# Performance work log

Hardware: AMD Instinct MI355X
Metric: run time of the kernel (lower is better)

The kernel has to match this reference:

```python
import jax, jax.numpy as jnp
import numpy as np

B = 65536
D_MODEL = 2048
N_EXPERTS = 64
TOP_K = 8
AUX_COEF = 0.01


def setup_inputs() -> dict:
    key = jax.random.key(0)
    kx, kw = jax.random.split(key)
    x = jax.random.normal(kx, (B, D_MODEL), dtype=jnp.float32)
    # nn.Linear(d_model, n_experts, bias=False); stored here as (d_model, n_experts)
    W = jax.random.normal(kw, (D_MODEL, N_EXPERTS), dtype=jnp.float32) / np.sqrt(D_MODEL).astype(np.float32)
    expert_bias = jnp.zeros((N_EXPERTS,), dtype=jnp.float32)
    return {"x": x, "W": W, "expert_bias": expert_bias}


def reference(x, W, expert_bias):
    # router logits: (B, n_experts)
    logits = x @ W
    # topk on bias-shifted logits (aux-loss-free balancing bias)
    biased = logits + expert_bias
    _, indices = jax.lax.top_k(biased, TOP_K)              # (B, top_k) int32
    # softmax over the UNbiased logits of the selected experts
    selected = jnp.take_along_axis(logits, indices, axis=-1)  # (B, top_k)
    gates_topk = jax.nn.softmax(selected, axis=-1)
    # scatter gate weights into sparse (B, n_experts) tensor
    rows = jnp.arange(logits.shape[0])[:, None]
    gates = jnp.zeros_like(logits).at[rows, indices].set(gates_topk)
    # aux load-balance loss (training mode): fraction routed * mean prob
    f_i = (gates > 0).astype(logits.dtype).mean(axis=0)       # (n_experts,)
    P_i = jax.nn.softmax(logits, axis=-1).mean(axis=0)        # (n_experts,)
    aux_loss = AUX_COEF * N_EXPERTS * jnp.sum(f_i * P_i)
    return gates, indices, aux_loss
```

## Files before the change

kernel.cpp:

```cpp
#include <hip/hip_runtime.h>
#include <cstdint>
#include <cstddef>

typedef __attribute__((ext_vector_type(8))) short short8;
typedef __attribute__((ext_vector_type(4))) float f32x4;

#define B_ROWS 65536
#define DMODEL 2048
#define NEXP 64
#define TOPK 8
#define THREADS 256
#define ROWS_PER_BLK 128
#define NBLK (B_ROWS / ROWS_PER_BLK)
#define NKS (DMODEL / 32)
#define SLAB 72
#define GOFF ((size_t)B_ROWS * NEXP)
#define AUX_OFF (GOFF + (size_t)B_ROWS * TOPK)
#define WS_FRAG_OFF 65536

__device__ __forceinline__ unsigned short bf16_rne(float v, float* back) {
  unsigned u = __float_as_uint(v);
  unsigned r = (u + 0x7FFFu + ((u >> 16) & 1u)) >> 16;
  *back = __uint_as_float(r << 16);
  return (unsigned short)r;
}

__global__ __launch_bounds__(256) void router_prep(
    const float* __restrict__ W, unsigned short* __restrict__ frag)
{
  const int ks = blockIdx.x;
  const int tid = threadIdx.x;
  const int nt = tid >> 6;
  const int lane = tid & 63;
  const int krow = ks * 32 + (lane >> 4) * 8;
  const int col = nt * 16 + (lane & 15);
  short8 hv, mv, lv;
#pragma unroll
  for (int j = 0; j < 8; ++j) {
    float v = W[(size_t)(krow + j) * NEXP + col];
    float fh, fm, fl;
    unsigned short h = bf16_rne(v, &fh);
    float r = v - fh;
    unsigned short m = bf16_rne(r, &fm);
    float r2 = r - fm;
    unsigned short l = bf16_rne(r2, &fl);
    hv[j] = (short)h; mv[j] = (short)m; lv[j] = (short)l;
  }
  size_t base = (size_t)(ks * 4 + nt) * 3 * 512 + lane * 8;
  *(short8*)(frag + base)        = hv;
  *(short8*)(frag + base + 512)  = mv;
  *(short8*)(frag + base + 1024) = lv;
}

__device__ __forceinline__ void cvt3(float4 a, float4 b,
                                     short8* H, short8* M, short8* L) {
  float f[8] = {a.x, a.y, a.z, a.w, b.x, b.y, b.z, b.w};
#pragma unroll
  for (int j = 0; j < 8; ++j) {
    float fh, fm, fl;
    unsigned short h = bf16_rne(f[j], &fh);
    float r = f[j] - fh;
    unsigned short m = bf16_rne(r, &fm);
    float r2 = r - fm;
    unsigned short l = bf16_rne(r2, &fl);
    (*H)[j] = (short)h; (*M)[j] = (short)m; (*L)[j] = (short)l;
  }
}

#define MFMA __builtin_amdgcn_mfma_f32_16x16x32_bf16

__global__ __launch_bounds__(THREADS, 2) void router_main(
    const float* __restrict__ x, const float* __restrict__ bias,
    const unsigned short* __restrict__ frag, float* __restrict__ out,
    float* __restrict__ ws)
{
  __shared__ __align__(16) float lds[ROWS_PER_BLK * SLAB + 256];

  const int tid = threadIdx.x;
  const int lane = tid & 63;
  const int w = tid >> 6;
  const size_t row0 = (size_t)blockIdx.x * ROWS_PER_BLK;

  f32x4 acc[2][4];
#pragma unroll
  for (int m = 0; m < 2; ++m)
#pragma unroll
    for (int nt = 0; nt < 4; ++nt) acc[m][nt] = (f32x4){0.f, 0.f, 0.f, 0.f};

  const float* xp0 = x + (row0 + (size_t)w * 32 + (lane & 15)) * DMODEL
                   + (lane >> 4) * 8;
  const float* xp1 = xp0 + (size_t)16 * DMODEL;
  const short8* fb = (const short8*)frag;

  for (int ks = 0; ks < NKS; ++ks) {
    float4 a00 = *(const float4*)(xp0 + ks * 32);
    float4 a01 = *(const float4*)(xp0 + ks * 32 + 4);
    float4 a10 = *(const float4*)(xp1 + ks * 32);
    float4 a11 = *(const float4*)(xp1 + ks * 32 + 4);
    short8 Bh[4], Bm[4], Bl[4];
#pragma unroll
    for (int nt = 0; nt < 4; ++nt) {
      size_t fb0 = (size_t)(ks * 4 + nt) * 3 * 64 + lane;
      Bh[nt] = fb[fb0];
      Bm[nt] = fb[fb0 + 64];
      Bl[nt] = fb[fb0 + 128];
    }
    short8 Ah0, Am0, Al0, Ah1, Am1, Al1;
    cvt3(a00, a01, &Ah0, &Am0, &Al0);
    cvt3(a10, a11, &Ah1, &Am1, &Al1);
#pragma unroll
    for (int nt = 0; nt < 4; ++nt) {
      acc[0][nt] = MFMA(Ah0, Bh[nt], acc[0][nt], 0, 0, 0);
      acc[0][nt] = MFMA(Ah0, Bm[nt], acc[0][nt], 0, 0, 0);
      acc[0][nt] = MFMA(Am0, Bh[nt], acc[0][nt], 0, 0, 0);
      acc[0][nt] = MFMA(Am0, Bm[nt], acc[0][nt], 0, 0, 0);
      acc[0][nt] = MFMA(Ah0, Bl[nt], acc[0][nt], 0, 0, 0);
      acc[0][nt] = MFMA(Al0, Bh[nt], acc[0][nt], 0, 0, 0);
      acc[1][nt] = MFMA(Ah1, Bh[nt], acc[1][nt], 0, 0, 0);
      acc[1][nt] = MFMA(Ah1, Bm[nt], acc[1][nt], 0, 0, 0);
      acc[1][nt] = MFMA(Am1, Bh[nt], acc[1][nt], 0, 0, 0);
      acc[1][nt] = MFMA(Am1, Bm[nt], acc[1][nt], 0, 0, 0);
      acc[1][nt] = MFMA(Ah1, Bl[nt], acc[1][nt], 0, 0, 0);
      acc[1][nt] = MFMA(Al1, Bh[nt], acc[1][nt], 0, 0, 0);
    }
  }

  float* slab = lds;
#pragma unroll
  for (int m = 0; m < 2; ++m)
#pragma unroll
    for (int nt = 0; nt < 4; ++nt)
#pragma unroll
      for (int reg = 0; reg < 4; ++reg) {
        int row = w * 32 + m * 16 + (lane >> 4) * 4 + reg;
        int col = nt * 16 + (lane & 15);
        slab[row * SLAB + col] = acc[m][nt][reg];
      }
  __syncthreads();

  float* redF = lds + ROWS_PER_BLK * SLAB;
  float* redP = redF + 128;

  if (w < 2) {
    const int row = w * 64 + lane;
    float a[NEXP];
#pragma unroll
    for (int n = 0; n < NEXP; ++n) a[n] = slab[row * SLAB + n];

    unsigned long long sel = 0ull;
    int idx[TOPK];
    float selu[TOPK];
#pragma unroll
    for (int k = 0; k < TOPK; ++k) {
      float best = -INFINITY, bestu = 0.f;
      int bi = 0;
#pragma unroll
      for (int n = 0; n < NEXP; ++n) {
        float vb = a[n] + bias[n];
        bool taken = (sel >> n) & 1ull;
        vb = taken ? -INFINITY : vb;
        if (vb > best) { best = vb; bestu = a[n]; bi = n; }
      }
      sel |= 1ull << bi;
      idx[k] = bi;
      selu[k] = bestu;
    }

    float mx = selu[0];
#pragma unroll
    for (int k = 1; k < TOPK; ++k) mx = fmaxf(mx, selu[k]);
    float g[TOPK]; float gs = 0.f;
#pragma unroll
    for (int k = 0; k < TOPK; ++k) { g[k] = __expf(selu[k] - mx); gs += g[k]; }
    float ginv = 1.f / gs;

    float* grow = out + (row0 + row) * NEXP;
#pragma unroll
    for (int n4 = 0; n4 < 16; ++n4) {
      float gv[4];
#pragma unroll
      for (int j = 0; j < 4; ++j) {
        int n = n4 * 4 + j;
        float v = 0.f;
#pragma unroll
        for (int k = 0; k < TOPK; ++k) v = (idx[k] == n) ? g[k] * ginv : v;
        gv[j] = v;
      }
      *(float4*)(grow + n4 * 4) = make_float4(gv[0], gv[1], gv[2], gv[3]);
    }

    float* irow = out + GOFF + (row0 + row) * TOPK;
    *(float4*)(irow + 0) = make_float4((float)idx[0], (float)idx[1], (float)idx[2], (float)idx[3]);
    *(float4*)(irow + 4) = make_float4((float)idx[4], (float)idx[5], (float)idx[6], (float)idx[7]);

    float m2 = -INFINITY;
#pragma unroll
    for (int n = 0; n < NEXP; ++n) m2 = fmaxf(m2, a[n]);
    float s2 = 0.f;
#pragma unroll
    for (int n = 0; n < NEXP; ++n) s2 += __expf(a[n] - m2);
    float pinv = 1.f / s2;

    float myP = 0.f, myF = 0.f;
#pragma unroll
    for (int n = 0; n < NEXP; ++n) {
      float v = __expf(a[n] - m2) * pinv;
      v += __shfl_xor(v, 1);
      v += __shfl_xor(v, 2);
      v += __shfl_xor(v, 4);
      v += __shfl_xor(v, 8);
      v += __shfl_xor(v, 16);
      v += __shfl_xor(v, 32);
      unsigned long long b = __ballot((sel >> n) & 1ull);
      if (lane == n) { myP = v; myF = (float)__popcll(b); }
    }
    redF[w * 64 + lane] = myF;
    redP[w * 64 + lane] = myP;
  }

  __syncthreads();
  if (tid < NEXP) {
    float F = redF[tid] + redF[64 + tid];
    float P = redP[tid] + redP[64 + tid];
    ws[(size_t)blockIdx.x * (2 * NEXP) + tid] = F;
    ws[(size_t)blockIdx.x * (2 * NEXP) + NEXP + tid] = P;
  }
}

__global__ __launch_bounds__(256) void router_aux(
    const float* __restrict__ ws, float* __restrict__ out)
{
  __shared__ float sf[4][NEXP];
  __shared__ float sp[4][NEXP];
  int t = threadIdx.x;
  int n = t & 63, part = t >> 6;
  float f = 0.f, p = 0.f;
#pragma unroll 8
  for (int b = part; b < NBLK; b += 4) {
    f += ws[(size_t)b * (2 * NEXP) + n];
    p += ws[(size_t)b * (2 * NEXP) + NEXP + n];
  }
  sf[part][n] = f;
  sp[part][n] = p;
  __syncthreads();
  if (t < NEXP) {
    float F = sf[0][t] + sf[1][t] + sf[2][t] + sf[3][t];
    float P = sp[0][t] + sp[1][t] + sp[2][t] + sp[3][t];
    float v = F * P;
    v += __shfl_xor(v, 1);
    v += __shfl_xor(v, 2);
    v += __shfl_xor(v, 4);
    v += __shfl_xor(v, 8);
    v += __shfl_xor(v, 16);
    v += __shfl_xor(v, 32);
    if (t == 0)
      out[AUX_OFF] = 0.01f * 64.f * v / (4294967296.0f );
  }
}

extern "C" void kernel_launch(void* const* d_in, const int* in_sizes, int n_in,
                              void* d_out, int out_size, void* d_ws, size_t ws_size,
                              hipStream_t stream) {
  const float* x = (const float*)d_in[0];
  const float* W = (const float*)d_in[1];
  const float* bias = (const float*)d_in[2];
  float* out = (float*)d_out;
  float* ws = (float*)d_ws;
  unsigned short* frag = (unsigned short*)(ws + WS_FRAG_OFF);
  router_prep<<<NKS, 256, 0, stream>>>(W, frag);
  router_main<<<NBLK, THREADS, 0, stream>>>(x, bias, frag, out, ws);
  router_aux<<<1, 256, 0, stream>>>(ws, out);
}
```

Before: 212.8 us.

## Stage B fragments in LDS via async global_load_lds with double buffering

Halves the rows per block to 64 so each wave handles 16 rows, and raises the occupancy target to 4 blocks per CU. The split-bf16 weight fragments are now copied into LDS with async global-to-LDS loads and double-buffered across k-steps, and the next x tile is prefetched into registers while the MFMAs run. The per-block aux reduction now writes directly from a single wave. This trades one barrier per k-step, and twice as many blocks each loading the full weight fragments, for more latency hiding and less register pressure.

```diff
diff --git a/kernel.cpp b/kernel.cpp
--- a/kernel.cpp
+++ b/kernel.cpp
@@ -10,13 +10,18 @@
 #define NEXP 64
 #define TOPK 8
 #define THREADS 256
-#define ROWS_PER_BLK 128
+#define ROWS_PER_BLK 64
 #define NBLK (B_ROWS / ROWS_PER_BLK)
 #define NKS (DMODEL / 32)
-#define SLAB 72
+#define SLAB 67
 #define GOFF ((size_t)B_ROWS * NEXP)
 #define AUX_OFF (GOFF + (size_t)B_ROWS * TOPK)
-#define WS_FRAG_OFF 65536
+#define WS_FRAG_OFF 131072
+
+#define GLOAD16(g, l)                                                      \
+  __builtin_amdgcn_global_load_lds(                                       \
+      (const __attribute__((address_space(1))) void*)(g),                 \
+      (__attribute__((address_space(3))) void*)(l), 16, 0, 0)
 
 __device__ __forceinline__ unsigned short bf16_rne(float v, float* back) {
   unsigned u = __float_as_uint(v);
@@ -29,9 +34,8 @@
     const float* __restrict__ W, unsigned short* __restrict__ frag)
 {
   const int ks = blockIdx.x;
-  const int tid = threadIdx.x;
-  const int nt = tid >> 6;
-  const int lane = tid & 63;
+  const int nt = threadIdx.x >> 6;
+  const int lane = threadIdx.x & 63;
   const int krow = ks * 32 + (lane >> 4) * 8;
   const int col = nt * 16 + (lane & 15);
   short8 hv, mv, lv;
@@ -46,7 +50,7 @@
     unsigned short l = bf16_rne(r2, &fl);
     hv[j] = (short)h; mv[j] = (short)m; lv[j] = (short)l;
   }
-  size_t base = (size_t)(ks * 4 + nt) * 3 * 512 + lane * 8;
+  size_t base = (size_t)(ks * 4 + nt) * 1536 + lane * 8;
   *(short8*)(frag + base)        = hv;
   *(short8*)(frag + base + 512)  = mv;
   *(short8*)(frag + base + 1024) = lv;
@@ -69,83 +73,79 @@
 
 #define MFMA __builtin_amdgcn_mfma_f32_16x16x32_bf16
 
-__global__ __launch_bounds__(THREADS, 2) void router_main(
+__global__ __launch_bounds__(THREADS, 4) void router_main(
     const float* __restrict__ x, const float* __restrict__ bias,
     const unsigned short* __restrict__ frag, float* __restrict__ out,
     float* __restrict__ ws)
 {
-  __shared__ __align__(16) float lds[ROWS_PER_BLK * SLAB + 256];
+  __shared__ __align__(16) float lds[6144];
 
   const int tid = threadIdx.x;
   const int lane = tid & 63;
   const int w = tid >> 6;
   const size_t row0 = (size_t)blockIdx.x * ROWS_PER_BLK;
 
-  f32x4 acc[2][4];
-#pragma unroll
-  for (int m = 0; m < 2; ++m)
-#pragma unroll
-    for (int nt = 0; nt < 4; ++nt) acc[m][nt] = (f32x4){0.f, 0.f, 0.f, 0.f};
-
-  const float* xp0 = x + (row0 + (size_t)w * 32 + (lane & 15)) * DMODEL
-                   + (lane >> 4) * 8;
-  const float* xp1 = xp0 + (size_t)16 * DMODEL;
-  const short8* fb = (const short8*)frag;
+  f32x4 acc[4];
+#pragma unroll
+  for (int nt = 0; nt < 4; ++nt) acc[nt] = (f32x4){0.f, 0.f, 0.f, 0.f};
+
+  const float* xp = x + (row0 + (size_t)w * 16 + (lane & 15)) * DMODEL
+                  + (lane >> 4) * 8;
+
+#define STAGE(KS, BUF)                                                     \
+  do {                                                                     \
+    _Pragma("unroll") for (int j = 0; j < 3; ++j)                          \
+      GLOAD16(frag + (size_t)(KS) * 6144 + (w * 3 + j) * 512 + lane * 8,   \
+              lds + (BUF) * 3072 + (w * 3 + j) * 256);                     \
+  } while (0)
+
+  STAGE(0, 0);
+  float4 c0 = *(const float4*)(xp);
+  float4 c1 = *(const float4*)(xp + 4);
 
   for (int ks = 0; ks < NKS; ++ks) {
-    float4 a00 = *(const float4*)(xp0 + ks * 32);
-    float4 a01 = *(const float4*)(xp0 + ks * 32 + 4);
-    float4 a10 = *(const float4*)(xp1 + ks * 32);
-    float4 a11 = *(const float4*)(xp1 + ks * 32 + 4);
-    short8 Bh[4], Bm[4], Bl[4];
+    __syncthreads();
+    float4 n0, n1;
+    if (ks + 1 < NKS) {
+      STAGE(ks + 1, (ks + 1) & 1);
+      n0 = *(const float4*)(xp + (ks + 1) * 32);
+      n1 = *(const float4*)(xp + (ks + 1) * 32 + 4);
+    }
+    const float* bb = lds + (ks & 1) * 3072;
+    short8 B[12];
+#pragma unroll
+    for (int f = 0; f < 12; ++f)
+      B[f] = *(const short8*)(bb + f * 256 + lane * 4);
+    short8 Ah, Am, Al;
+    cvt3(c0, c1, &Ah, &Am, &Al);
 #pragma unroll
     for (int nt = 0; nt < 4; ++nt) {
-      size_t fb0 = (size_t)(ks * 4 + nt) * 3 * 64 + lane;
-      Bh[nt] = fb[fb0];
-      Bm[nt] = fb[fb0 + 64];
-      Bl[nt] = fb[fb0 + 128];
-    }
-    short8 Ah0, Am0, Al0, Ah1, Am1, Al1;
-    cvt3(a00, a01, &Ah0, &Am0, &Al0);
-    cvt3(a10, a11, &Ah1, &Am1, &Al1);
-#pragma unroll
-    for (int nt = 0; nt < 4; ++nt) {
-      acc[0][nt] = MFMA(Ah0, Bh[nt], acc[0][nt], 0, 0, 0);
-      acc[0][nt] = MFMA(Ah0, Bm[nt], acc[0][nt], 0, 0, 0);
-      acc[0][nt] = MFMA(Am0, Bh[nt], acc[0][nt], 0, 0, 0);
-      acc[0][nt] = MFMA(Am0, Bm[nt], acc[0][nt], 0, 0, 0);
-      acc[0][nt] = MFMA(Ah0, Bl[nt], acc[0][nt], 0, 0, 0);
-      acc[0][nt] = MFMA(Al0, Bh[nt], acc[0][nt], 0, 0, 0);
-      acc[1][nt] = MFMA(Ah1, Bh[nt], acc[1][nt], 0, 0, 0);
-      acc[1][nt] = MFMA(Ah1, Bm[nt], acc[1][nt], 0, 0, 0);
-      acc[1][nt] = MFMA(Am1, Bh[nt], acc[1][nt], 0, 0, 0);
-      acc[1][nt] = MFMA(Am1, Bm[nt], acc[1][nt], 0, 0, 0);
-      acc[1][nt] = MFMA(Ah1, Bl[nt], acc[1][nt], 0, 0, 0);
-      acc[1][nt] = MFMA(Al1, Bh[nt], acc[1][nt], 0, 0, 0);
-    }
-  }
-
+      acc[nt] = MFMA(Ah, B[nt * 3 + 0], acc[nt], 0, 0, 0);
+      acc[nt] = MFMA(Ah, B[nt * 3 + 1], acc[nt], 0, 0, 0);
+      acc[nt] = MFMA(Am, B[nt * 3 + 0], acc[nt], 0, 0, 0);
+      acc[nt] = MFMA(Am, B[nt * 3 + 1], acc[nt], 0, 0, 0);
+      acc[nt] = MFMA(Ah, B[nt * 3 + 2], acc[nt], 0, 0, 0);
+      acc[nt] = MFMA(Al, B[nt * 3 + 0], acc[nt], 0, 0, 0);
+    }
+    if (ks + 1 < NKS) { c0 = n0; c1 = n1; }
+  }
+
+  __syncthreads();
   float* slab = lds;
 #pragma unroll
-  for (int m = 0; m < 2; ++m)
-#pragma unroll
-    for (int nt = 0; nt < 4; ++nt)
-#pragma unroll
-      for (int reg = 0; reg < 4; ++reg) {
-        int row = w * 32 + m * 16 + (lane >> 4) * 4 + reg;
-        int col = nt * 16 + (lane & 15);
-        slab[row * SLAB + col] = acc[m][nt][reg];
-      }
+  for (int nt = 0; nt < 4; ++nt)
+#pragma unroll
+    for (int reg = 0; reg < 4; ++reg) {
+      int row = w * 16 + (lane >> 4) * 4 + reg;
+      int col = nt * 16 + (lane & 15);
+      slab[row * SLAB + col] = acc[nt][reg];
+    }
   __syncthreads();
 
-  float* redF = lds + ROWS_PER_BLK * SLAB;
-  float* redP = redF + 128;
-
-  if (w < 2) {
-    const int row = w * 64 + lane;
+  if (w == 0) {
     float a[NEXP];
 #pragma unroll
-    for (int n = 0; n < NEXP; ++n) a[n] = slab[row * SLAB + n];
+    for (int n = 0; n < NEXP; ++n) a[n] = slab[lane * SLAB + n];
 
     unsigned long long sel = 0ull;
     int idx[TOPK];
@@ -174,7 +174,7 @@
     for (int k = 0; k < TOPK; ++k) { g[k] = __expf(selu[k] - mx); gs += g[k]; }
     float ginv = 1.f / gs;
 
-    float* grow = out + (row0 + row) * NEXP;
+    float* grow = out + (row0 + lane) * NEXP;
 #pragma unroll
     for (int n4 = 0; n4 < 16; ++n4) {
       float gv[4];
@@ -189,7 +189,7 @@
       *(float4*)(grow + n4 * 4) = make_float4(gv[0], gv[1], gv[2], gv[3]);
     }
 
-    float* irow = out + GOFF + (row0 + row) * TOPK;
+    float* irow = out + GOFF + (row0 + lane) * TOPK;
     *(float4*)(irow + 0) = make_float4((float)idx[0], (float)idx[1], (float)idx[2], (float)idx[3]);
     *(float4*)(irow + 4) = make_float4((float)idx[4], (float)idx[5], (float)idx[6], (float)idx[7]);
 
@@ -214,16 +214,8 @@
       unsigned long long b = __ballot((sel >> n) & 1ull);
       if (lane == n) { myP = v; myF = (float)__popcll(b); }
     }
-    redF[w * 64 + lane] = myF;
-    redP[w * 64 + lane] = myP;
-  }
-
-  __syncthreads();
-  if (tid < NEXP) {
-    float F = redF[tid] + redF[64 + tid];
-    float P = redP[tid] + redP[64 + tid];
-    ws[(size_t)blockIdx.x * (2 * NEXP) + tid] = F;
-    ws[(size_t)blockIdx.x * (2 * NEXP) + NEXP + tid] = P;
+    ws[(size_t)blockIdx.x * (2 * NEXP) + lane] = myF;
+    ws[(size_t)blockIdx.x * (2 * NEXP) + NEXP + lane] = myP;
   }
 }
 
```

Measured after the change: 216.2 us. No clear change (+1.6%).
